# Performance work log

Hardware: AMD Instinct MI355X
Metric: run time of the kernel (lower is better)

Reference implementation:

```python
import jax, jax.numpy as jnp
import numpy as np
import math

N_HEAD = 16
N_FEAT = 1024
D_K = N_FEAT // N_HEAD


def setup_inputs() -> dict:
    key = jax.random.key(0)
    k1, k2, k3, k4, k5, k6 = jax.random.split(key, 6)
    B, T1, T2 = 4, 2048, 2048
    query = jax.random.normal(k1, (B, T1, N_FEAT), dtype=jnp.float32)
    key_t = jax.random.normal(k2, (B, T2, N_FEAT), dtype=jnp.float32)
    value = jax.random.normal(k3, (B, T2, N_FEAT), dtype=jnp.float32)
    mask = jax.random.randint(k4, (B, 1, T2), 0, 2, dtype=jnp.int32)
    # linear_q parameters (torch nn.Linear: y = x @ W.T + b)
    bound = 1.0 / math.sqrt(N_FEAT)
    Wq = jax.random.uniform(k5, (N_FEAT, N_FEAT), minval=-bound, maxval=bound, dtype=jnp.float32)
    bq = jax.random.uniform(k6, (N_FEAT,), minval=-bound, maxval=bound, dtype=jnp.float32)
    return {"query": query, "key": key_t, "value": value, "mask": mask, "Wq": Wq, "bq": bq}


def reference(query, key, value, mask, Wq, bq):
    B, T1, _ = query.shape
    T2 = key.shape[1]
    # q gets a learned projection; k, v are just reshaped (faithful to source)
    q = (jnp.einsum('btf,gf->btg', query, Wq) + bq).reshape(B, T1, N_HEAD, D_K).transpose(0, 2, 1, 3)
    k = key.reshape(B, T2, N_HEAD, D_K).transpose(0, 2, 1, 3)
    v = value.reshape(B, T2, N_HEAD, D_K).transpose(0, 2, 1, 3)
    scores = jnp.einsum('bhqd,bhkd->bhqk', q, k) / math.sqrt(D_K)  # [B,H,T1,T2]
    m = (mask[:, None, :, :] == 0)  # [B,1,1or T1,T2] broadcast over heads
    min_value = jnp.finfo(scores.dtype).min
    scores = jnp.where(m, min_value, scores)
    attn = jax.nn.softmax(scores, axis=-1)
    attn = jnp.where(m, 0.0, attn)
    x = jnp.einsum('bhqk,bhkd->bhqd', attn, v)  # dropout rate = 0 (eval)
    return x.transpose(0, 2, 1, 3).reshape(B, T1, N_FEAT)
```

## Files before the change

kernel.cpp:

```cpp
#include <hip/hip_runtime.h>
#include <hip/hip_bf16.h>

#define GPTR(p) ((__attribute__((address_space(1))) void*)(p))
#define LPTR(p) ((__attribute__((address_space(3))) void*)(p))

typedef __attribute__((ext_vector_type(8))) short short8;
typedef __attribute__((ext_vector_type(4))) float f32x4;
typedef __attribute__((ext_vector_type(16))) float f32x16;
typedef unsigned short u16t;
typedef unsigned int u32t;

#define NHEAD 16
#define DK 64
#define NF 1024
#define BB 4
#define TT 2048
#define BT (BB * TT)

static __device__ __forceinline__ u16t f2bf(float f) {
  union { float f; unsigned u; } c; c.f = f;
  unsigned r = c.u + 0x7fffu + ((c.u >> 16) & 1u);
  return (u16t)(r >> 16);
}

static __device__ __forceinline__ u32t pkbf(float a, float b) {
  float2 ff; ff.x = a; ff.y = b;
  __hip_bfloat162 h2 = __float22bfloat162_rn(ff);
  u32t uu; __builtin_memcpy(&uu, &h2, 4);
  return uu;
}

__global__ void cvt_kernel(const float* __restrict__ src, u16t* __restrict__ dst, int n4) {
  int stride = gridDim.x * blockDim.x;
  for (int i = blockIdx.x * blockDim.x + threadIdx.x; i < n4; i += stride) {
    float4 f = reinterpret_cast<const float4*>(src)[i];
    ushort4 o;
    o.x = f2bf(f.x); o.y = f2bf(f.y); o.z = f2bf(f.z); o.w = f2bf(f.w);
    reinterpret_cast<ushort4*>(dst)[i] = o;
  }
}

__global__ void compact_kernel(const int* __restrict__ mask, int* __restrict__ idx,
                               int* __restrict__ cnt) {
  __shared__ int sc[256];
  const int b = blockIdx.x;
  const int t = threadIdx.x;
  const int* m = mask + b * TT;
  const int base = t * 8;
  int c = 0;
#pragma unroll
  for (int i = 0; i < 8; ++i) c += (m[base + i] != 0);
  sc[t] = c;
  __syncthreads();
  for (int off = 1; off < 256; off <<= 1) {
    int v = (t >= off) ? sc[t - off] : 0;
    __syncthreads();
    sc[t] += v;
    __syncthreads();
  }
  int pos = sc[t] - c;
  int* ib = idx + b * TT;
#pragma unroll
  for (int i = 0; i < 8; ++i)
    if (m[base + i] != 0) ib[pos++] = base + i;
  if (t == 255) {
    int tot = sc[255];
    cnt[b] = tot;
    int totp = (tot + 63) & ~63;
    if (totp < 64) totp = 64;
    for (int j = tot; j < totp; ++j) ib[j] = 0;
  }
}

__launch_bounds__(256, 1)
__global__ void qproj_kernel(const float* __restrict__ A, const u16t* __restrict__ W,
                             const float* __restrict__ bias, u16t* __restrict__ C) {
  __shared__ u16t As[128 * 64];
  __shared__ u16t Bs[128 * 64];
  const int tid = threadIdx.x;
  const int m0 = blockIdx.x * 128;
  const int n0 = blockIdx.y * 128;
  const int w = tid >> 6, lane = tid & 63;
  const int wr = (w >> 1) * 64, wc = (w & 1) * 64;
  const int g = lane >> 4, r = lane & 15;

  f32x4 acc[4][4] = {};

  float4 a0[4], a1[4];
#pragma unroll
  for (int i = 0; i < 4; ++i) {
    int c = i * 256 + tid;
    int row = c >> 3, slot = c & 7;
    int gs = slot ^ (row & 7);
    const float* src = A + (size_t)(m0 + row) * NF + gs * 8;
    a0[i] = *reinterpret_cast<const float4*>(src);
    a1[i] = *reinterpret_cast<const float4*>(src + 4);
  }

  for (int kb = 0; kb < NF; kb += 64) {
    __syncthreads();
#pragma unroll
    for (int i = 0; i < 4; ++i) {
      int c = i * 256 + tid;
      int row = c >> 3, slot = c & 7;
      int gs = slot ^ (row & 7);
      __builtin_amdgcn_global_load_lds(GPTR(W + (size_t)(n0 + row) * NF + kb + gs * 8),
                                       LPTR(Bs + c * 8), 16, 0, 0);
    }
#pragma unroll
    for (int i = 0; i < 4; ++i) {
      int c = i * 256 + tid;
      union { u32t u[4]; int4 i4; } kw;
      kw.u[0] = pkbf(a0[i].x, a0[i].y);
      kw.u[1] = pkbf(a0[i].z, a0[i].w);
      kw.u[2] = pkbf(a1[i].x, a1[i].y);
      kw.u[3] = pkbf(a1[i].z, a1[i].w);
      *reinterpret_cast<int4*>(reinterpret_cast<char*>(As) + c * 16) = kw.i4;
    }
    __syncthreads();
    if (kb + 64 < NF) {
#pragma unroll
      for (int i = 0; i < 4; ++i) {
        int c = i * 256 + tid;
        int row = c >> 3, slot = c & 7;
        int gs = slot ^ (row & 7);
        const float* src = A + (size_t)(m0 + row) * NF + kb + 64 + gs * 8;
        a0[i] = *reinterpret_cast<const float4*>(src);
        a1[i] = *reinterpret_cast<const float4*>(src + 4);
      }
    }
#pragma unroll
    for (int kk = 0; kk < 2; ++kk) {
      short8 af[4], bfr[4];
#pragma unroll
      for (int i = 0; i < 4; ++i) {
        int row = wr + i * 16 + r;
        int slot = (4 * kk + g) ^ (row & 7);
        af[i] = *reinterpret_cast<const short8*>(As + row * 64 + slot * 8);
      }
#pragma unroll
      for (int j = 0; j < 4; ++j) {
        int row = wc + j * 16 + r;
        int slot = (4 * kk + g) ^ (row & 7);
        bfr[j] = *reinterpret_cast<const short8*>(Bs + row * 64 + slot * 8);
      }
#pragma unroll
      for (int i = 0; i < 4; ++i)
#pragma unroll
        for (int j = 0; j < 4; ++j)
          acc[i][j] = __builtin_amdgcn_mfma_f32_16x16x32_bf16(af[i], bfr[j], acc[i][j], 0, 0, 0);
    }
  }
#pragma unroll
  for (int i = 0; i < 4; ++i)
#pragma unroll
    for (int j = 0; j < 4; ++j) {
      int grow = m0 + wr + i * 16 + 4 * g;
      int gcol = n0 + wc + j * 16 + r;
      float bv = bias[gcol];
#pragma unroll
      for (int reg = 0; reg < 4; ++reg)
        C[(size_t)(grow + reg) * NF + gcol] = f2bf((acc[i][j][reg] + bv) * 0.18033688f);
    }
}

__launch_bounds__(512, 2)
__global__ void attn_kernel(const u16t* __restrict__ Q, const float* __restrict__ K,
                            const float* __restrict__ V, const int* __restrict__ idx,
                            const int* __restrict__ cntArr, float* __restrict__ O) {
  __shared__ __attribute__((aligned(16))) char lds[32768];

  const int tid = threadIdx.x;
  const int lane = tid & 63;
  const int w = tid >> 6;
  const int qc = lane & 31;
  const int hi = lane >> 5;
  const int b = blockIdx.x >> 4, h = blockIdx.x & 15;
  const size_t bbase = (size_t)b * TT * NF;
  const int hoff = h * DK;
  const int qrow0 = blockIdx.y * 512 + w * 32;

  const int cnt = cntArr[b];
  int cntpad = (cnt + 63) & ~63;
  if (cntpad < 64) cntpad = 64;
  const int* ib = idx + b * TT;

  short8 qa[2][4];
#pragma unroll
  for (int qt = 0; qt < 2; ++qt)
#pragma unroll
    for (int t = 0; t < 4; ++t)
      qa[qt][t] = *reinterpret_cast<const short8*>(
          Q + bbase + (size_t)(qrow0 + 256 * qt + qc) * NF + hoff + 16 * t + 8 * hi);

  f32x16 oacc[2][2] = {};
  float lsumA = 0.f, lsumB = 0.f;

  const int srow = tid >> 3;
  const int ksg = (tid & 7) ^ ((srow + (srow >> 3)) & 7);
  const int Qv = tid >> 5, sub = (tid >> 4) & 1, dq = tid & 15;
  const int slotbase = Qv ^ (dq >> 2) ^ (4 * (dq & 3));
  const int wbase = 4 * dq * 128 + (slotbase << 3) + 4 * sub;

  const int P0 = (qc + (qc >> 3)) & 7;
  const int P1 = (P0 + 4) & 7;
  const int kB0 = qc * 128 + ((hi ^ P0) << 4);
  const int kB1 = qc * 128 + 4096 + ((hi ^ P1) << 4);
  const int g0 = hi ^ (qc & 15) ^ ((qc >> 4) & 3);
  const int vRb0 = qc * 128 + (g0 << 3);
  const int vRb1 = (qc + 32) * 128 + ((g0 ^ 2) << 3);

  float4 kf32a, kf32b, vf32a, vf32b;
  {
    int kj = ib[srow];
    const float* kp = K + bbase + (size_t)kj * NF + hoff + ksg * 8;
    kf32a = *reinterpret_cast<const float4*>(kp);
    kf32b = *reinterpret_cast<const float4*>(kp + 4);
    int vj0 = ib[4 * Qv + 2 * sub];
    int vj1 = ib[4 * Qv + 2 * sub + 1];
    vf32a = *reinterpret_cast<const float4*>(V + bbase + (size_t)vj0 * NF + hoff + 4 * dq);
    vf32b = *reinterpret_cast<const float4*>(V + bbase + (size_t)vj1 * NF + hoff + 4 * dq);
  }

  for (int t2 = 0; t2 < cntpad; t2 += 64) {
    const int cb = (t2 >> 6) & 1;
    const int kbb = cb * 8192;
    const int vbb = 16384 + cb * 8192;

    {
      union { u32t u[4]; int4 i4; } kw;
      kw.u[0] = pkbf(kf32a.x, kf32a.y);
      kw.u[1] = pkbf(kf32a.z, kf32a.w);
      kw.u[2] = pkbf(kf32b.x, kf32b.y);
      kw.u[3] = pkbf(kf32b.z, kf32b.w);
      *reinterpret_cast<int4*>(lds + kbb + tid * 16) = kw.i4;
    }
    {
      u32t p0 = pkbf(vf32a.x, vf32b.x);
      u32t p1 = pkbf(vf32a.y, vf32b.y);
      u32t p2 = pkbf(vf32a.z, vf32b.z);
      u32t p3 = pkbf(vf32a.w, vf32b.w);
      *reinterpret_cast<u32t*>(lds + vbb + (wbase ^ 0) + 0) = p0;
      *reinterpret_cast<u32t*>(lds + vbb + (wbase ^ 8) + 128) = p1;
      *reinterpret_cast<u32t*>(lds + vbb + (wbase ^ 16) + 256) = p2;
      *reinterpret_cast<u32t*>(lds + vbb + (wbase ^ 24) + 384) = p3;
    }
    asm volatile("s_waitcnt vmcnt(0) lgkmcnt(0)" ::: "memory");
    __builtin_amdgcn_s_barrier();

    if (t2 + 64 < cntpad) {
      int kj = ib[t2 + 64 + srow];
      const float* kp = K + bbase + (size_t)kj * NF + hoff + ksg * 8;
      kf32a = *reinterpret_cast<const float4*>(kp);
      kf32b = *reinterpret_cast<const float4*>(kp + 4);
      int vj0 = ib[t2 + 64 + 4 * Qv + 2 * sub];
      int vj1 = ib[t2 + 64 + 4 * Qv + 2 * sub + 1];
      vf32a = *reinterpret_cast<const float4*>(V + bbase + (size_t)vj0 * NF + hoff + 4 * dq);
      vf32b = *reinterpret_cast<const float4*>(V + bbase + (size_t)vj1 * NF + hoff + 4 * dq);
    }

    f32x16 bias0 = {}, bias1 = {};
    if (t2 + 64 > cnt) {
#pragma unroll
      for (int reg = 0; reg < 16; ++reg) {
        const int j = t2 + (reg & 3) + 8 * (reg >> 2) + 4 * hi;
        bias0[reg] = (j < cnt) ? 0.f : -10000.f;
        bias1[reg] = (j + 32 < cnt) ? 0.f : -10000.f;
      }
    }

    f32x16 sA0, sA1, sB0, sB1;
    {
      short8 kf0 = *reinterpret_cast<const short8*>(lds + kbb + kB0);
      short8 kf1 = *reinterpret_cast<const short8*>(lds + kbb + kB1);
      sA0 = __builtin_amdgcn_mfma_f32_32x32x16_bf16(kf0, qa[0][0], bias0, 0, 0, 0);
      sA1 = __builtin_amdgcn_mfma_f32_32x32x16_bf16(kf1, qa[0][0], bias1, 0, 0, 0);
      sB0 = __builtin_amdgcn_mfma_f32_32x32x16_bf16(kf0, qa[1][0], bias0, 0, 0, 0);
      sB1 = __builtin_amdgcn_mfma_f32_32x32x16_bf16(kf1, qa[1][0], bias1, 0, 0, 0);
    }
#pragma unroll
    for (int t = 1; t < 4; ++t) {
      short8 kf0 = *reinterpret_cast<const short8*>(lds + kbb + (kB0 ^ (t << 5)));
      short8 kf1 = *reinterpret_cast<const short8*>(lds + kbb + (kB1 ^ (t << 5)));
      sA0 = __builtin_amdgcn_mfma_f32_32x32x16_bf16(kf0, qa[0][t], sA0, 0, 0, 0);
      sA1 = __builtin_amdgcn_mfma_f32_32x32x16_bf16(kf1, qa[0][t], sA1, 0, 0, 0);
      sB0 = __builtin_amdgcn_mfma_f32_32x32x16_bf16(kf0, qa[1][t], sB0, 0, 0, 0);
      sB1 = __builtin_amdgcn_mfma_f32_32x32x16_bf16(kf1, qa[1][t], sB1, 0, 0, 0);
    }

#pragma unroll
    for (int t = 0; t < 4; ++t) {
      union { u32t u[4]; short8 s; } pA, pB;
      float eA = 0.f, eB = 0.f;
#pragma unroll
      for (int i = 0; i < 4; ++i) {
        const int reg = (t & 1) * 8 + 2 * i;
        float xa = __builtin_exp2f(t < 2 ? sA0[reg] : sA1[reg]);
        float xb = __builtin_exp2f(t < 2 ? sA0[reg + 1] : sA1[reg + 1]);
        float ya = __builtin_exp2f(t < 2 ? sB0[reg] : sB1[reg]);
        float yb = __builtin_exp2f(t < 2 ? sB0[reg + 1] : sB1[reg + 1]);
        eA += xa + xb; eB += ya + yb;
        pA.u[i] = pkbf(xa, xb);
        pB.u[i] = pkbf(ya, yb);
      }
      lsumA += eA; lsumB += eB;
      union { uint2 u2[2]; short8 s; } vf0, vf1;
      vf0.u2[0] = *reinterpret_cast<const uint2*>(lds + vbb + (vRb0 ^ ((4 * t) << 3)));
      vf0.u2[1] = *reinterpret_cast<const uint2*>(lds + vbb + (vRb0 ^ (((4 * t) ^ 2) << 3)));
      vf1.u2[0] = *reinterpret_cast<const uint2*>(lds + vbb + (vRb1 ^ ((4 * t) << 3)));
      vf1.u2[1] = *reinterpret_cast<const uint2*>(lds + vbb + (vRb1 ^ (((4 * t) ^ 2) << 3)));
      oacc[0][0] = __builtin_amdgcn_mfma_f32_32x32x16_bf16(pA.s, vf0.s, oacc[0][0], 0, 0, 0);
      oacc[0][1] = __builtin_amdgcn_mfma_f32_32x32x16_bf16(pA.s, vf1.s, oacc[0][1], 0, 0, 0);
      oacc[1][0] = __builtin_amdgcn_mfma_f32_32x32x16_bf16(pB.s, vf0.s, oacc[1][0], 0, 0, 0);
      oacc[1][1] = __builtin_amdgcn_mfma_f32_32x32x16_bf16(pB.s, vf1.s, oacc[1][1], 0, 0, 0);
    }
  }

#pragma unroll
  for (int qt = 0; qt < 2; ++qt) {
    float lsq = qt ? lsumB : lsumA;
    float lall = lsq + __shfl_xor(lsq, 32, 64);
    float linv = (lall > 0.f) ? (1.0f / lall) : 0.f;
#pragma unroll
    for (int reg = 0; reg < 16; ++reg) {
      const int crow = (reg & 3) + 8 * (reg >> 2) + 4 * hi;
      float rl = __shfl(linv, crow, 64);
      float* orow = O + bbase + (size_t)(qrow0 + 256 * qt + crow) * NF + hoff + qc;
      orow[0] = oacc[qt][0][reg] * rl;
      orow[32] = oacc[qt][1][reg] * rl;
    }
  }
}

extern "C" void kernel_launch(void* const* d_in, const int* in_sizes, int n_in,
                              void* d_out, int out_size, void* d_ws, size_t ws_size,
                              hipStream_t stream) {
  const float* query = (const float*)d_in[0];
  const float* key   = (const float*)d_in[1];
  const float* value = (const float*)d_in[2];
  const int*   mask  = (const int*)d_in[3];
  const float* Wq    = (const float*)d_in[4];
  const float* bq    = (const float*)d_in[5];
  float* out = (float*)d_out;

  u16t* ws = (u16t*)d_ws;
  u16t* wb = ws;
  u16t* qp = ws + (size_t)1024 * 1024;
  int* idx = (int*)(ws + (size_t)9 * 1024 * 1024);
  int* cnt = idx + BB * TT;

  compact_kernel<<<BB, 256, 0, stream>>>(mask, idx, cnt);
  cvt_kernel<<<1024, 256, 0, stream>>>(Wq, wb, (NF * NF) / 4);

  qproj_kernel<<<dim3(BT / 128, NF / 128), 256, 0, stream>>>(query, wb, bq, qp);
  attn_kernel<<<dim3(BB * NHEAD, TT / 512), 512, 0, stream>>>(qp, key, value, idx, cnt, out);
}
```

Before: 103.5 us.

## Fuse Wq bf16 conversion into qproj and halve query rows per attention block

Drops the separate cvt_kernel and has qproj load fp32 Wq and convert it to bf16 in registers before the LDS store, removing one launch and a round trip of the converted weight. The attention kernel now handles one 32-row query tile per wave instead of two, doubles the grid along T1 and raises launch bounds to four blocks per CU. This aims for better occupancy and fewer accumulator registers, but each K/V tile staged in LDS is reused by half as many queries, so K/V loads double.

```diff
diff --git a/kernel.cpp b/kernel.cpp
--- a/kernel.cpp
+++ b/kernel.cpp
@@ -28,16 +28,6 @@
   __hip_bfloat162 h2 = __float22bfloat162_rn(ff);
   u32t uu; __builtin_memcpy(&uu, &h2, 4);
   return uu;
-}
-
-__global__ void cvt_kernel(const float* __restrict__ src, u16t* __restrict__ dst, int n4) {
-  int stride = gridDim.x * blockDim.x;
-  for (int i = blockIdx.x * blockDim.x + threadIdx.x; i < n4; i += stride) {
-    float4 f = reinterpret_cast<const float4*>(src)[i];
-    ushort4 o;
-    o.x = f2bf(f.x); o.y = f2bf(f.y); o.z = f2bf(f.z); o.w = f2bf(f.w);
-    reinterpret_cast<ushort4*>(dst)[i] = o;
-  }
 }
 
 __global__ void compact_kernel(const int* __restrict__ mask, int* __restrict__ idx,
@@ -73,7 +63,7 @@
 }
 
 __launch_bounds__(256, 1)
-__global__ void qproj_kernel(const float* __restrict__ A, const u16t* __restrict__ W,
+__global__ void qproj_kernel(const float* __restrict__ A, const float* __restrict__ W,
                              const float* __restrict__ bias, u16t* __restrict__ C) {
   __shared__ u16t As[128 * 64];
   __shared__ u16t Bs[128 * 64];
@@ -86,27 +76,22 @@
 
   f32x4 acc[4][4] = {};
 
-  float4 a0[4], a1[4];
+  float4 a0[4], a1[4], w0[4], w1[4];
 #pragma unroll
   for (int i = 0; i < 4; ++i) {
     int c = i * 256 + tid;
     int row = c >> 3, slot = c & 7;
     int gs = slot ^ (row & 7);
-    const float* src = A + (size_t)(m0 + row) * NF + gs * 8;
-    a0[i] = *reinterpret_cast<const float4*>(src);
-    a1[i] = *reinterpret_cast<const float4*>(src + 4);
+    const float* srcA = A + (size_t)(m0 + row) * NF + gs * 8;
+    a0[i] = *reinterpret_cast<const float4*>(srcA);
+    a1[i] = *reinterpret_cast<const float4*>(srcA + 4);
+    const float* srcW = W + (size_t)(n0 + row) * NF + gs * 8;
+    w0[i] = *reinterpret_cast<const float4*>(srcW);
+    w1[i] = *reinterpret_cast<const float4*>(srcW + 4);
   }
 
   for (int kb = 0; kb < NF; kb += 64) {
     __syncthreads();
-#pragma unroll
-    for (int i = 0; i < 4; ++i) {
-      int c = i * 256 + tid;
-      int row = c >> 3, slot = c & 7;
-      int gs = slot ^ (row & 7);
-      __builtin_amdgcn_global_load_lds(GPTR(W + (size_t)(n0 + row) * NF + kb + gs * 8),
-                                       LPTR(Bs + c * 8), 16, 0, 0);
-    }
 #pragma unroll
     for (int i = 0; i < 4; ++i) {
       int c = i * 256 + tid;
@@ -116,6 +101,12 @@
       kw.u[2] = pkbf(a1[i].x, a1[i].y);
       kw.u[3] = pkbf(a1[i].z, a1[i].w);
       *reinterpret_cast<int4*>(reinterpret_cast<char*>(As) + c * 16) = kw.i4;
+      union { u32t u[4]; int4 i4; } ww;
+      ww.u[0] = pkbf(w0[i].x, w0[i].y);
+      ww.u[1] = pkbf(w0[i].z, w0[i].w);
+      ww.u[2] = pkbf(w1[i].x, w1[i].y);
+      ww.u[3] = pkbf(w1[i].z, w1[i].w);
+      *reinterpret_cast<int4*>(reinterpret_cast<char*>(Bs) + c * 16) = ww.i4;
     }
     __syncthreads();
     if (kb + 64 < NF) {
@@ -124,9 +115,12 @@
         int c = i * 256 + tid;
         int row = c >> 3, slot = c & 7;
         int gs = slot ^ (row & 7);
-        const float* src = A + (size_t)(m0 + row) * NF + kb + 64 + gs * 8;
-        a0[i] = *reinterpret_cast<const float4*>(src);
-        a1[i] = *reinterpret_cast<const float4*>(src + 4);
+        const float* srcA = A + (size_t)(m0 + row) * NF + kb + 64 + gs * 8;
+        a0[i] = *reinterpret_cast<const float4*>(srcA);
+        a1[i] = *reinterpret_cast<const float4*>(srcA + 4);
+        const float* srcW = W + (size_t)(n0 + row) * NF + kb + 64 + gs * 8;
+        w0[i] = *reinterpret_cast<const float4*>(srcW);
+        w1[i] = *reinterpret_cast<const float4*>(srcW + 4);
       }
     }
 #pragma unroll
@@ -164,7 +158,7 @@
     }
 }
 
-__launch_bounds__(512, 2)
+__launch_bounds__(512, 4)
 __global__ void attn_kernel(const u16t* __restrict__ Q, const float* __restrict__ K,
                             const float* __restrict__ V, const int* __restrict__ idx,
                             const int* __restrict__ cntArr, float* __restrict__ O) {
@@ -178,23 +172,21 @@
   const int b = blockIdx.x >> 4, h = blockIdx.x & 15;
   const size_t bbase = (size_t)b * TT * NF;
   const int hoff = h * DK;
-  const int qrow0 = blockIdx.y * 512 + w * 32;
+  const int qrow0 = blockIdx.y * 256 + w * 32;
 
   const int cnt = cntArr[b];
   int cntpad = (cnt + 63) & ~63;
   if (cntpad < 64) cntpad = 64;
   const int* ib = idx + b * TT;
 
-  short8 qa[2][4];
-#pragma unroll
-  for (int qt = 0; qt < 2; ++qt)
-#pragma unroll
-    for (int t = 0; t < 4; ++t)
-      qa[qt][t] = *reinterpret_cast<const short8*>(
-          Q + bbase + (size_t)(qrow0 + 256 * qt + qc) * NF + hoff + 16 * t + 8 * hi);
-
-  f32x16 oacc[2][2] = {};
-  float lsumA = 0.f, lsumB = 0.f;
+  short8 qa[4];
+#pragma unroll
+  for (int t = 0; t < 4; ++t)
+    qa[t] = *reinterpret_cast<const short8*>(
+        Q + bbase + (size_t)(qrow0 + qc) * NF + hoff + 16 * t + 8 * hi);
+
+  f32x16 oacc0 = {}, oacc1 = {};
+  float lsum = 0.f;
 
   const int srow = tid >> 3;
   const int ksg = (tid & 7) ^ ((srow + (srow >> 3)) & 7);
@@ -269,66 +261,53 @@
       }
     }
 
-    f32x16 sA0, sA1, sB0, sB1;
+    f32x16 s0, s1;
     {
       short8 kf0 = *reinterpret_cast<const short8*>(lds + kbb + kB0);
       short8 kf1 = *reinterpret_cast<const short8*>(lds + kbb + kB1);
-      sA0 = __builtin_amdgcn_mfma_f32_32x32x16_bf16(kf0, qa[0][0], bias0, 0, 0, 0);
-      sA1 = __builtin_amdgcn_mfma_f32_32x32x16_bf16(kf1, qa[0][0], bias1, 0, 0, 0);
-      sB0 = __builtin_amdgcn_mfma_f32_32x32x16_bf16(kf0, qa[1][0], bias0, 0, 0, 0);
-      sB1 = __builtin_amdgcn_mfma_f32_32x32x16_bf16(kf1, qa[1][0], bias1, 0, 0, 0);
+      s0 = __builtin_amdgcn_mfma_f32_32x32x16_bf16(kf0, qa[0], bias0, 0, 0, 0);
+      s1 = __builtin_amdgcn_mfma_f32_32x32x16_bf16(kf1, qa[0], bias1, 0, 0, 0);
     }
 #pragma unroll
     for (int t = 1; t < 4; ++t) {
       short8 kf0 = *reinterpret_cast<const short8*>(lds + kbb + (kB0 ^ (t << 5)));
       short8 kf1 = *reinterpret_cast<const short8*>(lds + kbb + (kB1 ^ (t << 5)));
-      sA0 = __builtin_amdgcn_mfma_f32_32x32x16_bf16(kf0, qa[0][t], sA0, 0, 0, 0);
-      sA1 = __builtin_amdgcn_mfma_f32_32x32x16_bf16(kf1, qa[0][t], sA1, 0, 0, 0);
-      sB0 = __builtin_amdgcn_mfma_f32_32x32x16_bf16(kf0, qa[1][t], sB0, 0, 0, 0);
-      sB1 = __builtin_amdgcn_mfma_f32_32x32x16_bf16(kf1, qa[1][t], sB1, 0, 0, 0);
+      s0 = __builtin_amdgcn_mfma_f32_32x32x16_bf16(kf0, qa[t], s0, 0, 0, 0);
+      s1 = __builtin_amdgcn_mfma_f32_32x32x16_bf16(kf1, qa[t], s1, 0, 0, 0);
     }
 
 #pragma unroll
     for (int t = 0; t < 4; ++t) {
-      union { u32t u[4]; short8 s; } pA, pB;
-      float eA = 0.f, eB = 0.f;
+      union { u32t u[4]; short8 s; } pa;
+      float eA = 0.f;
 #pragma unroll
       for (int i = 0; i < 4; ++i) {
         const int reg = (t & 1) * 8 + 2 * i;
-        float xa = __builtin_exp2f(t < 2 ? sA0[reg] : sA1[reg]);
-        float xb = __builtin_exp2f(t < 2 ? sA0[reg + 1] : sA1[reg + 1]);
-        float ya = __builtin_exp2f(t < 2 ? sB0[reg] : sB1[reg]);
-        float yb = __builtin_exp2f(t < 2 ? sB0[reg + 1] : sB1[reg + 1]);
-        eA += xa + xb; eB += ya + yb;
-        pA.u[i] = pkbf(xa, xb);
-        pB.u[i] = pkbf(ya, yb);
-      }
-      lsumA += eA; lsumB += eB;
+        float xa = __builtin_exp2f(t < 2 ? s0[reg] : s1[reg]);
+        float xb = __builtin_exp2f(t < 2 ? s0[reg + 1] : s1[reg + 1]);
+        eA += xa + xb;
+        pa.u[i] = pkbf(xa, xb);
+      }
+      lsum += eA;
       union { uint2 u2[2]; short8 s; } vf0, vf1;
       vf0.u2[0] = *reinterpret_cast<const uint2*>(lds + vbb + (vRb0 ^ ((4 * t) << 3)));
       vf0.u2[1] = *reinterpret_cast<const uint2*>(lds + vbb + (vRb0 ^ (((4 * t) ^ 2) << 3)));
       vf1.u2[0] = *reinterpret_cast<const uint2*>(lds + vbb + (vRb1 ^ ((4 * t) << 3)));
       vf1.u2[1] = *reinterpret_cast<const uint2*>(lds + vbb + (vRb1 ^ (((4 * t) ^ 2) << 3)));
-      oacc[0][0] = __builtin_amdgcn_mfma_f32_32x32x16_bf16(pA.s, vf0.s, oacc[0][0], 0, 0, 0);
-      oacc[0][1] = __builtin_amdgcn_mfma_f32_32x32x16_bf16(pA.s, vf1.s, oacc[0][1], 0, 0, 0);
-      oacc[1][0] = __builtin_amdgcn_mfma_f32_32x32x16_bf16(pB.s, vf0.s, oacc[1][0], 0, 0, 0);
-      oacc[1][1] = __builtin_amdgcn_mfma_f32_32x32x16_bf16(pB.s, vf1.s, oacc[1][1], 0, 0, 0);
-    }
-  }
-
-#pragma unroll
-  for (int qt = 0; qt < 2; ++qt) {
-    float lsq = qt ? lsumB : lsumA;
-    float lall = lsq + __shfl_xor(lsq, 32, 64);
-    float linv = (lall > 0.f) ? (1.0f / lall) : 0.f;
-#pragma unroll
-    for (int reg = 0; reg < 16; ++reg) {
-      const int crow = (reg & 3) + 8 * (reg >> 2) + 4 * hi;
-      float rl = __shfl(linv, crow, 64);
-      float* orow = O + bbase + (size_t)(qrow0 + 256 * qt + crow) * NF + hoff + qc;
-      orow[0] = oacc[qt][0][reg] * rl;
-      orow[32] = oacc[qt][1][reg] * rl;
-    }
+      oacc0 = __builtin_amdgcn_mfma_f32_32x32x16_bf16(pa.s, vf0.s, oacc0, 0, 0, 0);
+      oacc1 = __builtin_amdgcn_mfma_f32_32x32x16_bf16(pa.s, vf1.s, oacc1, 0, 0, 0);
+    }
+  }
+
+  float lall = lsum + __shfl_xor(lsum, 32, 64);
+  float linv = (lall > 0.f) ? (1.0f / lall) : 0.f;
+#pragma unroll
+  for (int reg = 0; reg < 16; ++reg) {
+    const int crow = (reg & 3) + 8 * (reg >> 2) + 4 * hi;
+    float rl = __shfl(linv, crow, 64);
+    float* orow = O + bbase + (size_t)(qrow0 + crow) * NF + hoff + qc;
+    orow[0] = oacc0[reg] * rl;
+    orow[32] = oacc1[reg] * rl;
   }
 }
 
@@ -344,14 +323,12 @@
   float* out = (float*)d_out;
 
   u16t* ws = (u16t*)d_ws;
-  u16t* wb = ws;
-  u16t* qp = ws + (size_t)1024 * 1024;
-  int* idx = (int*)(ws + (size_t)9 * 1024 * 1024);
+  u16t* qp = ws;
+  int* idx = (int*)(ws + (size_t)8 * 1024 * 1024);
   int* cnt = idx + BB * TT;
 
   compact_kernel<<<BB, 256, 0, stream>>>(mask, idx, cnt);
-  cvt_kernel<<<1024, 256, 0, stream>>>(Wq, wb, (NF * NF) / 4);
-
-  qproj_kernel<<<dim3(BT / 128, NF / 128), 256, 0, stream>>>(query, wb, bq, qp);
-  attn_kernel<<<dim3(BB * NHEAD, TT / 512), 512, 0, stream>>>(qp, key, value, idx, cnt, out);
-}
+
+  qproj_kernel<<<dim3(BT / 128, NF / 128), 256, 0, stream>>>(query, Wq, bq, qp);
+  attn_kernel<<<dim3(BB * NHEAD, TT / 256), 512, 0, stream>>>(qp, key, value, idx, cnt, out);
+}
```

Measured after the change: 127.8 us. +23.5%, slower.
